# Performance work log

Measured on AMD Instinct MI355X. Metric: run time of the kernel, lower is better.

Reference implementation:

```python
import jax, jax.numpy as jnp
import numpy as np
from jax import lax

B, T, D, H = 512, 1024, 64, 128


def setup_inputs() -> dict:
    key = jax.random.key(0)
    ks = jax.random.split(key, 8)
    x = jax.random.normal(ks[0], (B, T, D), dtype=jnp.float32)
    # binary keep-mask (float, like torch where mask multiplies h)
    mask = (jax.random.uniform(ks[1], (B, T)) < 0.9).astype(jnp.float32)
    s_ih = 1.0 / np.sqrt(H)
    w_ih = jax.random.uniform(ks[2], (3 * H, D), minval=-s_ih, maxval=s_ih, dtype=jnp.float32)
    w_hh = jax.random.uniform(ks[3], (3 * H, H), minval=-s_ih, maxval=s_ih, dtype=jnp.float32)
    b_ih = jax.random.uniform(ks[4], (3 * H,), minval=-s_ih, maxval=s_ih, dtype=jnp.float32)
    b_hh = jax.random.uniform(ks[5], (3 * H,), minval=-s_ih, maxval=s_ih, dtype=jnp.float32)
    Wo = jax.random.normal(ks[6], (2, H), dtype=jnp.float32) * 0.1
    bo = jnp.zeros((2,), dtype=jnp.float32)
    return {"x": x, "mask": mask, "w_ih": w_ih, "w_hh": w_hh,
            "b_ih": b_ih, "b_hh": b_hh, "Wo": Wo, "bo": bo}


def reference(x, mask, w_ih, w_hh, b_ih, b_hh, Wo, bo):
    # Precompute input-side gate projections for all timesteps: [B,T,3H]
    xg_all = jnp.einsum('btd,gd->btg', x, w_ih) + b_ih

    def step(h, inp):
        xg, m = inp                     # xg: [B,3H], m: [B]
        hg = h @ w_hh.T + b_hh          # [B,3H]
        xr, xz, xn = jnp.split(xg, 3, axis=-1)
        hr, hz, hn = jnp.split(hg, 3, axis=-1)
        r = jax.nn.sigmoid(xr + hr)
        z = jax.nn.sigmoid(xz + hz)
        n = jnp.tanh(xn + r * hn)
        h_new = (1.0 - z) * n + z * h   # torch GRUCell update
        m = m[:, None]
        h = m * h_new + (1.0 - m) * h   # mask blend
        logit = h @ Wo.T + bo           # [B,2]
        return h, logit

    h0 = jnp.zeros((x.shape[0], w_hh.shape[1]), dtype=x.dtype)
    _, logits = lax.scan(step, h0, (jnp.swapaxes(xg_all, 0, 1), mask.T))
    return jnp.swapaxes(logits, 0, 1)   # [B,T,2]
```

## Files before the change

kernel.cpp:

```cpp
#include <hip/hip_runtime.h>

#define TB 512
#define TT 1024
#define TD 64
#define TH 128
#define NR 4

typedef __attribute__((ext_vector_type(8))) short short8;
typedef __attribute__((ext_vector_type(4))) float f32x4;
typedef __attribute__((ext_vector_type(2))) float f32x2;

#define LOG2E 1.44269504f

__device__ __forceinline__ short bfb(float f) {
    unsigned u = __builtin_bit_cast(unsigned, f);
    u = (u + 0x7FFFu + ((u >> 16) & 1u)) >> 16;
    return (short)u;
}

#define BAR() asm volatile("s_waitcnt lgkmcnt(0)\n\ts_barrier" ::: "memory")

#define MFMA(a, b, cc) __builtin_amdgcn_mfma_f32_16x16x32_bf16(a, b, cc, 0, 0, 0)

__device__ __forceinline__ float ext4(f32x4 v, bool s0, bool s1) {
    float a = s0 ? v[1] : v[0];
    float b = s0 ? v[3] : v[2];
    return s1 ? b : a;
}

__global__ __launch_bounds__(256)
void xswz(const float* __restrict__ x, short8* __restrict__ ws) {
    int gid = blockIdx.x * 256 + threadIdx.x;
    int e   = gid & 15;
    int kt  = (gid >> 4) & 1;
    int t   = (gid >> 5) & (TT - 1);
    int blk = gid >> 15;
    int c = e >> 2, quad = e & 3;
    const float* p = x + ((size_t)(blk * NR + c) * TT + t) * TD + 32 * kt + 8 * quad;
    f32x4 a = *(const f32x4*)p;
    f32x4 b = *(const f32x4*)(p + 4);
    short8 f;
    #pragma unroll
    for (int j = 0; j < 4; ++j) { f[j] = bfb(a[j]); f[4 + j] = bfb(b[j]); }
    ws[gid] = f;
}

template <bool USE_WS>
__global__ __launch_bounds__(512, 1)
void gru_mfma(const float* __restrict__ x, const short8* __restrict__ xw,
              const float* __restrict__ mask,
              const float* __restrict__ w_ih, const float* __restrict__ w_hh,
              const float* __restrict__ b_ih, const float* __restrict__ b_hh,
              const float* __restrict__ Wo, const float* __restrict__ bo,
              float* __restrict__ out)
{
    __shared__ short hbuf[2][4][144];
    __shared__ float mlds[TT][NR];

    const int tid  = threadIdx.x;
    const int w    = tid >> 6;
    const int lane = tid & 63;
    const int c    = lane & 15;
    const int quad = lane >> 4;
    const int Bb   = blockIdx.x * NR;
    const int cb   = c & 3;
    const bool s0  = ((c >> 2) & 1) != 0;
    const bool s1  = ((c >> 3) & 1) != 0;

    for (int i = tid; i < TT * NR; i += 512) {
        int t = i >> 2, b = i & 3;
        mlds[t][b] = mask[(size_t)(Bb + b) * TT + t];
    }
    for (int i = tid; i < 2 * 4 * 144; i += 512) (&hbuf[0][0][0])[i] = 0;

    const int jj = 16 * w + c;

    short8 whh[3][4], wih[3][2], wof[4];
    {
        const int gg[3] = {jj, TH + jj, 2 * TH + jj};
        #pragma unroll
        for (int g = 0; g < 3; ++g) {
            #pragma unroll
            for (int kt = 0; kt < 4; ++kt) {
                const float* p = w_hh + (size_t)gg[g] * TH + 32 * kt + 8 * quad;
                short8 f;
                #pragma unroll
                for (int j = 0; j < 8; ++j) f[j] = bfb(p[j]);
                whh[g][kt] = f;
            }
            #pragma unroll
            for (int kt = 0; kt < 2; ++kt) {
                const float* p = w_ih + (size_t)gg[g] * TD + 32 * kt + 8 * quad;
                short8 f;
                #pragma unroll
                for (int j = 0; j < 8; ++j) f[j] = bfb(p[j]);
                wih[g][kt] = f;
            }
        }
        #pragma unroll
        for (int kt = 0; kt < 4; ++kt) {
            short8 f = {0,0,0,0,0,0,0,0};
            if (c < 2) {
                const float* p = Wo + (size_t)c * TH + 32 * kt + 8 * quad;
                #pragma unroll
                for (int j = 0; j < 8; ++j) f[j] = bfb(p[j]);
            }
            wof[kt] = f;
        }
    }

    const int myc = 16 * w + 4 * quad + (c >> 2);
    const float crK = -LOG2E * (b_ih[myc] + b_hh[myc]);
    const float czK = -LOG2E * (b_ih[TH + myc] + b_hh[TH + myc]);
    const float bin = b_ih[2 * TH + myc];
    const float bhn = b_hh[2 * TH + myc];
    const float b0o = bo[0], b1o = bo[1];

    const short8 z8  = {0,0,0,0,0,0,0,0};
    const f32x4  zf4 = {0.f, 0.f, 0.f, 0.f};

    const short8* xwp  = xw + (size_t)blockIdx.x * (TT * 32) + (cb * 4 + quad);
    const float*  xrow = x + (size_t)(Bb + cb) * TT * TD + 8 * quad;

    short8 xf0[2], xf1[2];
    if (USE_WS) {
        xf0[0] = xwp[0];
        xf0[1] = xwp[16];
    } else {
        #pragma unroll
        for (int kt = 0; kt < 2; ++kt) {
            f32x4 a = *(const f32x4*)(xrow + 32 * kt);
            f32x4 b = *(const f32x4*)(xrow + 32 * kt + 4);
            short8 f;
            #pragma unroll
            for (int j = 0; j < 4; ++j) { f[j] = bfb(a[j]); f[4 + j] = bfb(b[j]); }
            xf0[kt] = f;
        }
    }

    f32x4 xacA[3], xacB[3];
    #pragma unroll
    for (int g = 0; g < 3; ++g) {
        f32x4 a = zf4;
        a = MFMA(wih[g][0], xf0[0], a);
        a = MFMA(wih[g][1], xf0[1], a);
        xacA[g] = a;
    }

    if (USE_WS) {
        xf0[0] = xwp[32];
        xf0[1] = xwp[48];
    } else {
        const float* p = xrow + (size_t)1 * TD;
        #pragma unroll
        for (int kt = 0; kt < 2; ++kt) {
            f32x4 a = *(const f32x4*)(p + 32 * kt);
            f32x4 b = *(const f32x4*)(p + 32 * kt + 4);
            short8 f;
            #pragma unroll
            for (int j = 0; j < 4; ++j) { f[j] = bfb(a[j]); f[4 + j] = bfb(b[j]); }
            xf0[kt] = f;
        }
    }

    float hold = 0.0f;

#define STEP(T, XC, XN, AC, AN)                                                 \
  {                                                                             \
    const int t = (T);                                                          \
    BAR();                                                                      \
    const int rb = t & 1, wb = rb ^ 1;                                          \
    short8 ha[4];                                                               \
    _Pragma("unroll")                                                           \
    for (int kt = 0; kt < 4; ++kt)                                              \
        ha[kt] = *(const short8*)(&hbuf[rb][cb][32 * kt + 8 * quad]);           \
    const float m = mlds[t][cb];           \
    const int tn = (t + 2 < TT) ? t + 2 : TT - 1;                               \
    f32x4 nxa0, nxb0, nxa1, nxb1;                                               \
    if (USE_WS) {                                                               \
        XN[0] = xwp[(size_t)tn * 32];                                           \
        XN[1] = xwp[(size_t)tn * 32 + 16];                                      \
    } else {                                                                    \
        const float* p = xrow + (size_t)tn * TD;                                \
        nxa0 = *(const f32x4*)(p);      nxb0 = *(const f32x4*)(p + 4);          \
        nxa1 = *(const f32x4*)(p + 32); nxb1 = *(const f32x4*)(p + 36);         \
    }                                                                           \
                          \
    f32x4 rA = AC[0], zA = AC[1], nA = zf4;                                     \
    f32x4 rB = zf4, zB = zf4, nB = zf4;                                         \
    rA = MFMA(whh[0][0], ha[0], rA);                                            \
    zA = MFMA(whh[1][0], ha[0], zA);                                            \
    nA = MFMA(whh[2][0], ha[0], nA);                                            \
    rB = MFMA(whh[0][2], ha[2], rB);                                            \
    zB = MFMA(whh[1][2], ha[2], zB);                                            \
    nB = MFMA(whh[2][2], ha[2], nB);                                            \
    rA = MFMA(whh[0][1], ha[1], rA);                                            \
    zA = MFMA(whh[1][1], ha[1], zA);                                            \
    nA = MFMA(whh[2][1], ha[1], nA);                                            \
    rB = MFMA(whh[0][3], ha[3], rB);                                            \
    zB = MFMA(whh[1][3], ha[3], zB);                                            \
    nB = MFMA(whh[2][3], ha[3], nB);                                            \
           \
    if (t > 0 && w == ((t - 1) & 7)) {                                          \
        f32x4 lacc = zf4;                                                       \
        _Pragma("unroll")                                                       \
        for (int kt = 0; kt < 4; ++kt) lacc = MFMA(wof[kt], ha[kt], lacc);      \
        if (quad == 0 && c < 4) {                                               \
            f32x2 lo = {lacc[0] + b0o, lacc[1] + b1o};                          \
            *(f32x2*)(out + ((size_t)(Bb + c) * TT + (t - 1)) * 2) = lo;        \
        }                                                                       \
    }                                                                           \
              \
    _Pragma("unroll")                                                           \
    for (int g = 0; g < 3; ++g) {                                               \
        f32x4 a = zf4;                                                          \
        a = MFMA(wih[g][0], XC[0], a);                                          \
        a = MFMA(wih[g][1], XC[1], a);                                          \
        AN[g] = a;                                                              \
    }                                                                           \
               \
    {                                                                           \
        float arS  = ext4(rA + rB, s0, s1);                                     \
        float azS  = ext4(zA + zB, s0, s1);                                     \
        float anhS = ext4(nA + nB, s0, s1);                                     \
        float anxS = ext4(AC[2],   s0, s1);                                     \
        float er = __builtin_amdgcn_exp2f(__builtin_fmaf(arS, -LOG2E, crK));    \
        float r  = __builtin_amdgcn_rcpf(1.0f + er);                            \
        float ez = __builtin_amdgcn_exp2f(__builtin_fmaf(azS, -LOG2E, czK));    \
        float z  = __builtin_amdgcn_rcpf(1.0f + ez);                            \
        float pp = (anxS + bin) + r * (anhS + bhn);                             \
        float e2 = __builtin_amdgcn_exp2f(pp * (2.0f * LOG2E));                 \
        float n  = __builtin_fmaf(-2.0f, __builtin_amdgcn_rcpf(1.0f + e2), 1.0f); \
        float hn = n + z * (hold - n);                                          \
        hold = hold + m * (hn - hold);                                          \
        hbuf[wb][cb][myc] = bfb(hold);                                          \
    }                                                                           \
    if (!USE_WS) {                                                              \
        short8 f0, f1;                                                          \
        _Pragma("unroll")                                                       \
        for (int j = 0; j < 4; ++j) { f0[j] = bfb(nxa0[j]); f0[4+j] = bfb(nxb0[j]); \
                                      f1[j] = bfb(nxa1[j]); f1[4+j] = bfb(nxb1[j]); } \
        XN[0] = f0; XN[1] = f1;                                                 \
    }                                                                           \
  }

    for (int t2 = 0; t2 < TT; t2 += 2) {
        STEP(t2,     xf0, xf1, xacA, xacB);
        STEP(t2 + 1, xf1, xf0, xacB, xacA);
    }
#undef STEP

    BAR();
    if (w == 7) {
        short8 ha[4];
        #pragma unroll
        for (int kt = 0; kt < 4; ++kt)
            ha[kt] = *(const short8*)(&hbuf[0][cb][32 * kt + 8 * quad]);
        f32x4 lacc = zf4;
        #pragma unroll
        for (int kt = 0; kt < 4; ++kt) lacc = MFMA(wof[kt], ha[kt], lacc);
        if (quad == 0 && c < 4) {
            f32x2 lo = {lacc[0] + b0o, lacc[1] + b1o};
            *(f32x2*)(out + ((size_t)(Bb + c) * TT + (TT - 1)) * 2) = lo;
        }
    }
}

extern "C" void kernel_launch(void* const* d_in, const int* in_sizes, int n_in,
                              void* d_out, int out_size, void* d_ws, size_t ws_size,
                              hipStream_t stream) {
    const float* x    = (const float*)d_in[0];
    const float* mask = (const float*)d_in[1];
    const float* w_ih = (const float*)d_in[2];
    const float* w_hh = (const float*)d_in[3];
    const float* b_ih = (const float*)d_in[4];
    const float* b_hh = (const float*)d_in[5];
    const float* Wo   = (const float*)d_in[6];
    const float* bo   = (const float*)d_in[7];
    float* out = (float*)d_out;
    (void)in_sizes; (void)n_in; (void)out_size;

    const size_t nfrag = (size_t)(TB / NR) * TT * 2 * 16;
    const size_t need  = nfrag * sizeof(short8);
    if (ws_size >= need) {
        short8* xw = (short8*)d_ws;
        xswz<<<(int)(nfrag / 256), 256, 0, stream>>>(x, xw);
        gru_mfma<true><<<TB / NR, 512, 0, stream>>>(x, xw, mask, w_ih, w_hh,
                                                    b_ih, b_hh, Wo, bo, out);
    } else {
        gru_mfma<false><<<TB / NR, 512, 0, stream>>>(x, (const short8*)nullptr, mask,
                                                     w_ih, w_hh, b_ih, b_hh, Wo, bo, out);
    }
}
```

Baseline: 740.4 us.

## Halve block to 4 waves, each computing two hidden-column tiles per step

Each block now runs 4 waves instead of 8. Every wave owns 32 hidden units split into two interleaved 16-column MFMA tiles, so it issues twice the MFMAs per step. Each lane writes two packed bf16 hidden values with one 32-bit LDS store. The aim is to cut barrier cost and wave synchronisation on the serial recurrence. In exchange, each wave has twice the weight registers and a longer MFMA chain per step, which adds register pressure and per-step latency.

```diff
diff --git a/kernel.cpp b/kernel.cpp
--- a/kernel.cpp
+++ b/kernel.cpp
@@ -46,7 +46,7 @@
 }
 
 template <bool USE_WS>
-__global__ __launch_bounds__(512, 1)
+__global__ __launch_bounds__(256, 1)
 void gru_mfma(const float* __restrict__ x, const short8* __restrict__ xw,
               const float* __restrict__ mask,
               const float* __restrict__ w_ih, const float* __restrict__ w_hh,
@@ -67,17 +67,17 @@
     const bool s0  = ((c >> 2) & 1) != 0;
     const bool s1  = ((c >> 3) & 1) != 0;
 
-    for (int i = tid; i < TT * NR; i += 512) {
+    for (int i = tid; i < TT * NR; i += 256) {
         int t = i >> 2, b = i & 3;
         mlds[t][b] = mask[(size_t)(Bb + b) * TT + t];
     }
-    for (int i = tid; i < 2 * 4 * 144; i += 512) (&hbuf[0][0][0])[i] = 0;
-
-    const int jj = 16 * w + c;
-
-    short8 whh[3][4], wih[3][2], wof[4];
-    {
-        const int gg[3] = {jj, TH + jj, 2 * TH + jj};
+    for (int i = tid; i < 2 * 4 * 144; i += 256) (&hbuf[0][0][0])[i] = 0;
+
+    short8 whh2[2][3][4], wih2[2][3][2], wof[4];
+    #pragma unroll
+    for (int T = 0; T < 2; ++T) {
+        const int jjT = 32 * w + 2 * c + T;
+        const int gg[3] = {jjT, TH + jjT, 2 * TH + jjT};
         #pragma unroll
         for (int g = 0; g < 3; ++g) {
             #pragma unroll
@@ -86,7 +86,7 @@
                 short8 f;
                 #pragma unroll
                 for (int j = 0; j < 8; ++j) f[j] = bfb(p[j]);
-                whh[g][kt] = f;
+                whh2[T][g][kt] = f;
             }
             #pragma unroll
             for (int kt = 0; kt < 2; ++kt) {
@@ -94,30 +94,34 @@
                 short8 f;
                 #pragma unroll
                 for (int j = 0; j < 8; ++j) f[j] = bfb(p[j]);
-                wih[g][kt] = f;
+                wih2[T][g][kt] = f;
             }
         }
-        #pragma unroll
-        for (int kt = 0; kt < 4; ++kt) {
-            short8 f = {0,0,0,0,0,0,0,0};
-            if (c < 2) {
-                const float* p = Wo + (size_t)c * TH + 32 * kt + 8 * quad;
-                #pragma unroll
-                for (int j = 0; j < 8; ++j) f[j] = bfb(p[j]);
-            }
-            wof[kt] = f;
-        }
-    }
-
-    const int myc = 16 * w + 4 * quad + (c >> 2);
-    const float crK = -LOG2E * (b_ih[myc] + b_hh[myc]);
-    const float czK = -LOG2E * (b_ih[TH + myc] + b_hh[TH + myc]);
-    const float bin = b_ih[2 * TH + myc];
-    const float bhn = b_hh[2 * TH + myc];
+    }
+    #pragma unroll
+    for (int kt = 0; kt < 4; ++kt) {
+        short8 f = {0,0,0,0,0,0,0,0};
+        if (c < 2) {
+            const float* p = Wo + (size_t)c * TH + 32 * kt + 8 * quad;
+            #pragma unroll
+            for (int j = 0; j < 8; ++j) f[j] = bfb(p[j]);
+        }
+        wof[kt] = f;
+    }
+
+    const int colL = 32 * w + 8 * quad + 2 * (c >> 2);
+    float crK[2], czK[2], binc[2], bhnc[2];
+    #pragma unroll
+    for (int T = 0; T < 2; ++T) {
+        const int mc = colL + T;
+        crK[T]  = -LOG2E * (b_ih[mc] + b_hh[mc]);
+        czK[T]  = -LOG2E * (b_ih[TH + mc] + b_hh[TH + mc]);
+        binc[T] = b_ih[2 * TH + mc];
+        bhnc[T] = b_hh[2 * TH + mc];
+    }
     const float b0o = bo[0], b1o = bo[1];
 
-    const short8 z8  = {0,0,0,0,0,0,0,0};
-    const f32x4  zf4 = {0.f, 0.f, 0.f, 0.f};
+    const f32x4 zf4 = {0.f, 0.f, 0.f, 0.f};
 
     const short8* xwp  = xw + (size_t)blockIdx.x * (TT * 32) + (cb * 4 + quad);
     const float*  xrow = x + (size_t)(Bb + cb) * TT * TD + 8 * quad;
@@ -138,14 +142,16 @@
         }
     }
 
-    f32x4 xacA[3], xacB[3];
-    #pragma unroll
-    for (int g = 0; g < 3; ++g) {
-        f32x4 a = zf4;
-        a = MFMA(wih[g][0], xf0[0], a);
-        a = MFMA(wih[g][1], xf0[1], a);
-        xacA[g] = a;
-    }
+    f32x4 xacA[2][3], xacB[2][3];
+    #pragma unroll
+    for (int T = 0; T < 2; ++T)
+        #pragma unroll
+        for (int g = 0; g < 3; ++g) {
+            f32x4 a = zf4;
+            a = MFMA(wih2[T][g][0], xf0[0], a);
+            a = MFMA(wih2[T][g][1], xf0[1], a);
+            xacA[T][g] = a;
+        }
 
     if (USE_WS) {
         xf0[0] = xwp[32];
@@ -163,11 +169,11 @@
         }
     }
 
-    float hold = 0.0f;
-
-#define STEP(T, XC, XN, AC, AN)                                                 \
+    f32x2 hold2 = {0.f, 0.f};
+
+#define STEP(T_, XC, XN, AC, AN)                                                \
   {                                                                             \
-    const int t = (T);                                                          \
+    const int t = (T_);                                                         \
     BAR();                                                                      \
     const int rb = t & 1, wb = rb ^ 1;                                          \
     short8 ha[4];                                                               \
@@ -185,23 +191,37 @@
         nxa0 = *(const f32x4*)(p);      nxb0 = *(const f32x4*)(p + 4);          \
         nxa1 = *(const f32x4*)(p + 32); nxb1 = *(const f32x4*)(p + 36);         \
     }                                                                           \
-                          \
-    f32x4 rA = AC[0], zA = AC[1], nA = zf4;                                     \
-    f32x4 rB = zf4, zB = zf4, nB = zf4;                                         \
-    rA = MFMA(whh[0][0], ha[0], rA);                                            \
-    zA = MFMA(whh[1][0], ha[0], zA);                                            \
-    nA = MFMA(whh[2][0], ha[0], nA);                                            \
-    rB = MFMA(whh[0][2], ha[2], rB);                                            \
-    zB = MFMA(whh[1][2], ha[2], zB);                                            \
-    nB = MFMA(whh[2][2], ha[2], nB);                                            \
-    rA = MFMA(whh[0][1], ha[1], rA);                                            \
-    zA = MFMA(whh[1][1], ha[1], zA);                                            \
-    nA = MFMA(whh[2][1], ha[1], nA);                                            \
-    rB = MFMA(whh[0][3], ha[3], rB);                                            \
-    zB = MFMA(whh[1][3], ha[3], zB);                                            \
-    nB = MFMA(whh[2][3], ha[3], nB);                                            \
+       \
+    f32x4 r0A = AC[0][0], z0A = AC[0][1], n0A = zf4;                            \
+    f32x4 r1A = AC[1][0], z1A = AC[1][1], n1A = zf4;                            \
+    f32x4 r0B = zf4, z0B = zf4, n0B = zf4;                                      \
+    f32x4 r1B = zf4, z1B = zf4, n1B = zf4;                                      \
+    r0A = MFMA(whh2[0][0][0], ha[0], r0A);                                      \
+    z0A = MFMA(whh2[0][1][0], ha[0], z0A);                                      \
+    n0A = MFMA(whh2[0][2][0], ha[0], n0A);                                      \
+    r1A = MFMA(whh2[1][0][0], ha[0], r1A);                                      \
+    z1A = MFMA(whh2[1][1][0], ha[0], z1A);                                      \
+    n1A = MFMA(whh2[1][2][0], ha[0], n1A);                                      \
+    r0B = MFMA(whh2[0][0][2], ha[2], r0B);                                      \
+    z0B = MFMA(whh2[0][1][2], ha[2], z0B);                                      \
+    n0B = MFMA(whh2[0][2][2], ha[2], n0B);                                      \
+    r1B = MFMA(whh2[1][0][2], ha[2], r1B);                                      \
+    z1B = MFMA(whh2[1][1][2], ha[2], z1B);                                      \
+    n1B = MFMA(whh2[1][2][2], ha[2], n1B);                                      \
+    r0A = MFMA(whh2[0][0][1], ha[1], r0A);                                      \
+    z0A = MFMA(whh2[0][1][1], ha[1], z0A);                                      \
+    n0A = MFMA(whh2[0][2][1], ha[1], n0A);                                      \
+    r1A = MFMA(whh2[1][0][1], ha[1], r1A);                                      \
+    z1A = MFMA(whh2[1][1][1], ha[1], z1A);                                      \
+    n1A = MFMA(whh2[1][2][1], ha[1], n1A);                                      \
+    r0B = MFMA(whh2[0][0][3], ha[3], r0B);                                      \
+    z0B = MFMA(whh2[0][1][3], ha[3], z0B);                                      \
+    n0B = MFMA(whh2[0][2][3], ha[3], n0B);                                      \
+    r1B = MFMA(whh2[1][0][3], ha[3], r1B);                                      \
+    z1B = MFMA(whh2[1][1][3], ha[3], z1B);                                      \
+    n1B = MFMA(whh2[1][2][3], ha[3], n1B);                                      \
            \
-    if (t > 0 && w == ((t - 1) & 7)) {                                          \
+    if (t > 0 && w == ((t - 1) & 3)) {                                          \
         f32x4 lacc = zf4;                                                       \
         _Pragma("unroll")                                                       \
         for (int kt = 0; kt < 4; ++kt) lacc = MFMA(wof[kt], ha[kt], lacc);      \
@@ -212,28 +232,45 @@
     }                                                                           \
               \
     _Pragma("unroll")                                                           \
-    for (int g = 0; g < 3; ++g) {                                               \
-        f32x4 a = zf4;                                                          \
-        a = MFMA(wih[g][0], XC[0], a);                                          \
-        a = MFMA(wih[g][1], XC[1], a);                                          \
-        AN[g] = a;                                                              \
-    }                                                                           \
-               \
+    for (int Tt = 0; Tt < 2; ++Tt)                                              \
+        _Pragma("unroll")                                                       \
+        for (int g = 0; g < 3; ++g) {                                           \
+            f32x4 a = zf4;                                                      \
+            a = MFMA(wih2[Tt][g][0], XC[0], a);                                 \
+            a = MFMA(wih2[Tt][g][1], XC[1], a);                                 \
+            AN[Tt][g] = a;                                                      \
+        }                                                                       \
+       \
     {                                                                           \
-        float arS  = ext4(rA + rB, s0, s1);                                     \
-        float azS  = ext4(zA + zB, s0, s1);                                     \
-        float anhS = ext4(nA + nB, s0, s1);                                     \
-        float anxS = ext4(AC[2],   s0, s1);                                     \
-        float er = __builtin_amdgcn_exp2f(__builtin_fmaf(arS, -LOG2E, crK));    \
-        float r  = __builtin_amdgcn_rcpf(1.0f + er);                            \
-        float ez = __builtin_amdgcn_exp2f(__builtin_fmaf(azS, -LOG2E, czK));    \
-        float z  = __builtin_amdgcn_rcpf(1.0f + ez);                            \
-        float pp = (anxS + bin) + r * (anhS + bhn);                             \
-        float e2 = __builtin_amdgcn_exp2f(pp * (2.0f * LOG2E));                 \
-        float n  = __builtin_fmaf(-2.0f, __builtin_amdgcn_rcpf(1.0f + e2), 1.0f); \
-        float hn = n + z * (hold - n);                                          \
-        hold = hold + m * (hn - hold);                                          \
-        hbuf[wb][cb][myc] = bfb(hold);                                          \
+        float arS0  = ext4(r0A + r0B, s0, s1);                                  \
+        float azS0  = ext4(z0A + z0B, s0, s1);                                  \
+        float anhS0 = ext4(n0A + n0B, s0, s1);                                  \
+        float anxS0 = ext4(AC[0][2],  s0, s1);                                  \
+        float arS1  = ext4(r1A + r1B, s0, s1);                                  \
+        float azS1  = ext4(z1A + z1B, s0, s1);                                  \
+        float anhS1 = ext4(n1A + n1B, s0, s1);                                  \
+        float anxS1 = ext4(AC[1][2],  s0, s1);                                  \
+        float er0 = __builtin_amdgcn_exp2f(__builtin_fmaf(arS0, -LOG2E, crK[0])); \
+        float er1 = __builtin_amdgcn_exp2f(__builtin_fmaf(arS1, -LOG2E, crK[1])); \
+        float r0  = __builtin_amdgcn_rcpf(1.0f + er0);                          \
+        float r1  = __builtin_amdgcn_rcpf(1.0f + er1);                          \
+        float ez0 = __builtin_amdgcn_exp2f(__builtin_fmaf(azS0, -LOG2E, czK[0])); \
+        float ez1 = __builtin_amdgcn_exp2f(__builtin_fmaf(azS1, -LOG2E, czK[1])); \
+        float z0  = __builtin_amdgcn_rcpf(1.0f + ez0);                          \
+        float z1  = __builtin_amdgcn_rcpf(1.0f + ez1);                          \
+        float pp0 = (anxS0 + binc[0]) + r0 * (anhS0 + bhnc[0]);                 \
+        float pp1 = (anxS1 + binc[1]) + r1 * (anhS1 + bhnc[1]);                 \
+        float e20 = __builtin_amdgcn_exp2f(pp0 * (2.0f * LOG2E));               \
+        float e21 = __builtin_amdgcn_exp2f(pp1 * (2.0f * LOG2E));               \
+        float n0  = __builtin_fmaf(-2.0f, __builtin_amdgcn_rcpf(1.0f + e20), 1.0f); \
+        float n1  = __builtin_fmaf(-2.0f, __builtin_amdgcn_rcpf(1.0f + e21), 1.0f); \
+        float hn0 = n0 + z0 * (hold2[0] - n0);                                  \
+        float hn1 = n1 + z1 * (hold2[1] - n1);                                  \
+        hold2[0] = hold2[0] + m * (hn0 - hold2[0]);                             \
+        hold2[1] = hold2[1] + m * (hn1 - hold2[1]);                             \
+        unsigned pk = (unsigned)(unsigned short)bfb(hold2[0]) |                 \
+                      ((unsigned)(unsigned short)bfb(hold2[1]) << 16);          \
+        *(unsigned*)(&hbuf[wb][cb][colL]) = pk;                                 \
     }                                                                           \
     if (!USE_WS) {                                                              \
         short8 f0, f1;                                                          \
@@ -251,7 +288,7 @@
 #undef STEP
 
     BAR();
-    if (w == 7) {
+    if (w == 3) {
         short8 ha[4];
         #pragma unroll
         for (int kt = 0; kt < 4; ++kt)
@@ -285,10 +322,10 @@
     if (ws_size >= need) {
         short8* xw = (short8*)d_ws;
         xswz<<<(int)(nfrag / 256), 256, 0, stream>>>(x, xw);
-        gru_mfma<true><<<TB / NR, 512, 0, stream>>>(x, xw, mask, w_ih, w_hh,
+        gru_mfma<true><<<TB / NR, 256, 0, stream>>>(x, xw, mask, w_ih, w_hh,
                                                     b_ih, b_hh, Wo, bo, out);
     } else {
-        gru_mfma<false><<<TB / NR, 512, 0, stream>>>(x, (const short8*)nullptr, mask,
+        gru_mfma<false><<<TB / NR, 256, 0, stream>>>(x, (const short8*)nullptr, mask,
                                                      w_ih, w_hh, b_ih, b_hh, Wo, bo, out);
     }
 }
```

Measured after the change: 887.0 us. +19.8%, slower.
